# Performance work log

Measured on AMD Instinct MI355X. Metric: run time of the kernel, lower is better.

The kernel has to match this reference:

```python
import jax, jax.numpy as jnp
from jax import lax
import numpy as np

DIM = 1024
SEQ = 2048
BATCH = 2
DEPTH = 2
D_INNER = 2 * DIM          # expand=2
D_STATE = 16
D_CONV = 4
DT_RANK = DIM // 16        # ceil(dim/16) = 64
FF = 4 * DIM               # ff_mult=4
EPS = 1e-5


def rmsnorm(x, w, eps=EPS):
    return x * lax.rsqrt(jnp.mean(x * x, axis=-1, keepdims=True) + eps) * w


def layernorm(x, w, b, eps=EPS):
    mu = jnp.mean(x, axis=-1, keepdims=True)
    var = jnp.mean((x - mu) ** 2, axis=-1, keepdims=True)
    return (x - mu) * lax.rsqrt(var + eps) * w + b


def silu(x):
    return x * jax.nn.sigmoid(x)


def causal_conv1d(x, w, b):
    # x: [b, l, d], depthwise causal conv, kernel w: [d, k], bias b: [d]
    xc = jnp.transpose(x, (0, 2, 1))  # [b, d, l]
    y = lax.conv_general_dilated(
        xc, w[:, None, :], window_strides=(1,), padding=[(D_CONV - 1, 0)],
        dimension_numbers=("NCH", "OIH", "NCH"), feature_group_count=D_INNER)
    y = y + b[None, :, None]
    return jnp.transpose(y, (0, 2, 1))  # [b, l, d]


def selective_scan(u, delta, A, B, C, D):
    # u, delta: [b, l, d]; A: [d, n]; B, C: [b, l, n]; D: [d]
    def step(h, inp):
        d_t, b_t, c_t, u_t = inp                       # [b,d],[b,n],[b,n],[b,d]
        dA = jnp.exp(d_t[..., None] * A)               # [b, d, n]
        h = dA * h + (d_t * u_t)[..., None] * b_t[:, None, :]
        y = jnp.einsum("bdn,bn->bd", h, c_t)
        return h, y

    h0 = jnp.zeros((u.shape[0], A.shape[0], A.shape[1]), u.dtype)
    xs = (jnp.swapaxes(delta, 0, 1), jnp.swapaxes(B, 0, 1),
          jnp.swapaxes(C, 0, 1), jnp.swapaxes(u, 0, 1))
    _, ys = lax.scan(step, h0, xs)                     # ys: [l, b, d]
    return jnp.swapaxes(ys, 0, 1) + u * D


def mamba_mixer(h, in_w, cw, cb, xp_w, dtp_w, dtp_b, A_log, D, out_w):
    # h: [b, l, dim]
    xz = jnp.einsum("bld,ed->ble", h, in_w)            # [b, l, 2*d_inner]
    x_in, z = jnp.split(xz, 2, axis=-1)
    x_c = silu(causal_conv1d(x_in, cw, cb))            # [b, l, d_inner]
    x_dbl = jnp.einsum("ble,re->blr", x_c, xp_w)       # [b, l, dt_rank+2n]
    dt = x_dbl[..., :DT_RANK]
    B = x_dbl[..., DT_RANK:DT_RANK + D_STATE]
    C = x_dbl[..., DT_RANK + D_STATE:]
    delta = jax.nn.softplus(jnp.einsum("blr,er->ble", dt, dtp_w) + dtp_b)
    A = -jnp.exp(A_log)
    y = selective_scan(x_c, delta, A, B, C, D)
    y = y * silu(z)
    return jnp.einsum("ble,de->bld", y, out_w)         # [b, l, dim]


def setup_inputs() -> dict:
    key = jax.random.key(0)
    ks = jax.random.split(key, 16)

    def nrm(k, shape, s=0.02):
        return jax.random.normal(k, shape, dtype=jnp.float32) * s

    A_init = jnp.log(jnp.tile(jnp.arange(1, D_STATE + 1, dtype=jnp.float32),
                              (DEPTH, D_INNER, 1)))
    return {
        "x": jax.random.normal(ks[0], (BATCH, SEQ, DIM), jnp.float32),
        "in_proj_w": nrm(ks[1], (DEPTH, 2 * D_INNER, DIM)),
        "conv_w": nrm(ks[2], (DEPTH, D_INNER, D_CONV), 0.1),
        "conv_b": jnp.zeros((DEPTH, D_INNER), jnp.float32),
        "x_proj_w": nrm(ks[3], (DEPTH, DT_RANK + 2 * D_STATE, D_INNER)),
        "dt_proj_w": nrm(ks[4], (DEPTH, D_INNER, DT_RANK), 0.1),
        "dt_proj_b": nrm(ks[5], (DEPTH, D_INNER), 0.1),
        "A_log": A_init,
        "D": jnp.ones((DEPTH, D_INNER), jnp.float32),
        "out_proj_w": nrm(ks[6], (DEPTH, DIM, D_INNER)),
        "rms_w": jnp.ones((DEPTH, DIM), jnp.float32),
        "ln_w": jnp.ones((DEPTH, DIM), jnp.float32),
        "ln_b": jnp.zeros((DEPTH, DIM), jnp.float32),
        "ff_w1": nrm(ks[7], (2 * FF, DIM)),
        "ff_b1": jnp.zeros((2 * FF,), jnp.float32),
        "ff_w2": nrm(ks[8], (DIM, FF)),
        "ff_b2": jnp.zeros((DIM,), jnp.float32),
    }


def reference(x, in_proj_w, conv_w, conv_b, x_proj_w, dt_proj_w, dt_proj_b,
              A_log, D, out_proj_w, rms_w, ln_w, ln_b, ff_w1, ff_b1, ff_w2, ff_b2):
    residual = None
    h = x
    for i in range(in_proj_w.shape[0]):
        # fused add + RMSNorm (prenorm, residual in fp32)
        residual = h if residual is None else residual + h
        normed = rmsnorm(residual, rms_w[i])
        h = mamba_mixer(normed, in_proj_w[i], conv_w[i], conv_b[i],
                        x_proj_w[i], dt_proj_w[i], dt_proj_b[i],
                        A_log[i], D[i], out_proj_w[i])
        # extra per-block LayerNorm on mixer output
        h = layernorm(h, ln_w[i], ln_b[i])
    # final GEGLU feedforward
    u = jnp.einsum("bld,ed->ble", h, ff_w1) + ff_b1    # [b, l, 2*FF]
    a, g = jnp.split(u, 2, axis=-1)
    v = a * jax.nn.gelu(g, approximate=False)
    return jnp.einsum("blf,df->bld", v, ff_w2) + ff_b2
```

## Files before the change

### kernel.cpp

```cpp
#include <hip/hip_runtime.h>
#include <cstdint>
#include <cstddef>

#define DIM     1024
#define SEQ     2048
#define BATCH   2
#define DEPTH   2
#define D_INNER 2048
#define D_STATE 16
#define D_CONV  4
#define DT_RANK 64
#define FF      4096
#define ROWS    (BATCH*SEQ)
#define EPS     1e-5f

#define CS      32
#define NC      (SEQ/CS)
#define NC_LOG  6

#define XP_KS    8
#define XP_KSTEP (D_INNER/XP_KS)

#define LOG2E 1.44269504088896f

typedef unsigned short ushort_t;
typedef short bf16x8 __attribute__((ext_vector_type(8)));
typedef float f32x4  __attribute__((ext_vector_type(4)));

__device__ __forceinline__ float sigmoidf_(float x) { return 1.f / (1.f + __expf(-x)); }

__device__ __forceinline__ ushort_t f2bf(float x) {
  unsigned int u = __float_as_uint(x);
  u += 0x7fffu + ((u >> 16) & 1u);
  return (ushort_t)(u >> 16);
}
__device__ __forceinline__ float bf2f(ushort_t u) {
  return __uint_as_float((unsigned)u << 16);
}

__device__ __forceinline__ void async_cp16(const void* g, void* lds) {
  __builtin_amdgcn_global_load_lds(
      (const __attribute__((address_space(1))) unsigned int*)g,
      (__attribute__((address_space(3))) unsigned int*)lds, 16, 0, 0);
}

__device__ __forceinline__ float2 block_sum2(float a, float b) {
#pragma unroll
  for (int off = 32; off > 0; off >>= 1) {
    a += __shfl_down(a, off, 64);
    b += __shfl_down(b, off, 64);
  }
  __shared__ float sa[4], sb[4];
  __syncthreads();
  if ((threadIdx.x & 63) == 0) { int w = threadIdx.x >> 6; sa[w] = a; sb[w] = b; }
  __syncthreads();
  return make_float2(sa[0] + sa[1] + sa[2] + sa[3], sb[0] + sb[1] + sb[2] + sb[3]);
}

__global__ __launch_bounds__(256) void res_rms_kernel(
    const float* __restrict__ xin,
    float* __restrict__ res, ushort_t* __restrict__ nrm, const float* __restrict__ w) {
  int row = blockIdx.x;
  const float* xr = xin + (size_t)row * DIM;
  float* rr = res + (size_t)row * DIM;
  ushort_t* nr = nrm + (size_t)row * DIM;
  float v[4]; float ss = 0.f;
#pragma unroll
  for (int i = 0; i < 4; ++i) {
    int j = threadIdx.x + i * 256;
    float t = xr[j];
    v[i] = t; rr[j] = t; ss += t * t;
  }
  float2 s = block_sum2(ss, 0.f);
  float rstd = rsqrtf(s.x * (1.f / DIM) + EPS);
#pragma unroll
  for (int i = 0; i < 4; ++i) {
    int j = threadIdx.x + i * 256;
    nr[j] = f2bf(v[i] * rstd * w[j]);
  }
}

__global__ __launch_bounds__(256) void ln_res_rms_kernel(
    const float* __restrict__ in, float* __restrict__ res,
    const float* __restrict__ lw, const float* __restrict__ lb,
    const float* __restrict__ rw, ushort_t* __restrict__ nrm) {
  int row = blockIdx.x;
  const float* xr = in + (size_t)row * DIM;
  float* rr = res + (size_t)row * DIM;
  ushort_t* nr = nrm + (size_t)row * DIM;
  float v[4]; float s1 = 0.f, s2 = 0.f;
#pragma unroll
  for (int i = 0; i < 4; ++i) {
    int j = threadIdx.x + i * 256;
    float t = xr[j];
    v[i] = t; s1 += t; s2 += t * t;
  }
  float2 s = block_sum2(s1, s2);
  float mean = s.x * (1.f / DIM);
  float var = s.y * (1.f / DIM) - mean * mean;
  float rstd = rsqrtf(var + EPS);
  float t4[4]; float ss = 0.f;
#pragma unroll
  for (int i = 0; i < 4; ++i) {
    int j = threadIdx.x + i * 256;
    float o = (v[i] - mean) * rstd * lw[j] + lb[j];
    float t = rr[j] + o;
    rr[j] = t;
    t4[i] = t; ss += t * t;
  }
  float2 s2v = block_sum2(ss, 0.f);
  float rstd2 = rsqrtf(s2v.x * (1.f / DIM) + EPS);
#pragma unroll
  for (int i = 0; i < 4; ++i) {
    int j = threadIdx.x + i * 256;
    nr[j] = f2bf(t4[i] * rstd2 * rw[j]);
  }
}

__global__ __launch_bounds__(256) void ln_final_kernel(
    const float* __restrict__ in, ushort_t* __restrict__ outb,
    const float* __restrict__ w, const float* __restrict__ b) {
  int row = blockIdx.x;
  const float* xr = in + (size_t)row * DIM;
  ushort_t* obrow = outb + (size_t)row * DIM;
  float v[4]; float s1 = 0.f, s2 = 0.f;
#pragma unroll
  for (int i = 0; i < 4; ++i) {
    int j = threadIdx.x + i * 256;
    float t = xr[j];
    v[i] = t; s1 += t; s2 += t * t;
  }
  float2 s = block_sum2(s1, s2);
  float mean = s.x * (1.f / DIM);
  float var = s.y * (1.f / DIM) - mean * mean;
  float rstd = rsqrtf(var + EPS);
#pragma unroll
  for (int i = 0; i < 4; ++i) {
    int j = threadIdx.x + i * 256;
    obrow[j] = f2bf((v[i] - mean) * rstd * w[j] + b[j]);
  }
}

__global__ __launch_bounds__(256) void f2b_all(
    const float* __restrict__ w0, ushort_t* __restrict__ d0,
    const float* __restrict__ w1, ushort_t* __restrict__ d1,
    const float* __restrict__ w2, ushort_t* __restrict__ d2,
    const float* __restrict__ w3, ushort_t* __restrict__ d3) {
  int i = (blockIdx.x * 256 + threadIdx.x) * 4;
  const float* s; ushort_t* d; int off;
  if (i < 8388608)        { s = w0; d = d0; off = i; }
  else if (i < 12582912)  { s = w1; d = d1; off = i - 8388608; }
  else if (i < 20971520)  { s = w2; d = d2; off = i - 12582912; }
  else                    { s = w3; d = d3; off = i - 20971520; }
  float4 v = *reinterpret_cast<const float4*>(s + off);
  d[off + 0] = f2bf(v.x); d[off + 1] = f2bf(v.y);
  d[off + 2] = f2bf(v.z); d[off + 3] = f2bf(v.w);
}

__global__ __launch_bounds__(256) void gemm_bf16_nt(
    const ushort_t* __restrict__ A,
    const ushort_t* __restrict__ B,
    float* __restrict__ C,
    ushort_t* __restrict__ Cb,
    int N, int K,
    const float* __restrict__ bias, int grp) {
  __shared__ ushort_t As[2][128 * 64];
  __shared__ ushort_t Bs[2][128 * 64];
  const int tid = threadIdx.x;
  const int l = tid & 63;
  const int w = tid >> 6;

  const unsigned nwgx = gridDim.x;
  const unsigned nwg = nwgx * gridDim.y;
  const unsigned bid = blockIdx.y * nwgx + blockIdx.x;
  const unsigned cpx = nwg >> 3;
  const unsigned s = (bid & 7u) * cpx + (bid >> 3);
  const unsigned bandw = (unsigned)grp * nwgx;
  const unsigned band = s / bandw;
  const unsigned rem = s % bandw;
  const int m0 = (int)(band * grp + (rem % grp)) * 128;
  const int n0 = (int)(rem / grp) * 128;

  const int wm = (w >> 1) * 64;
  const int wn = (w & 1) * 64;

  const int srow = l >> 3;
  const int ksrc = 8 * ((l & 7) ^ srow);
  const int kg = l >> 4;
  const int lr = l & 15;

  f32x4 acc[4][4];
#pragma unroll
  for (int mi = 0; mi < 4; ++mi)
#pragma unroll
    for (int ni = 0; ni < 4; ++ni) acc[mi][ni] = (f32x4)0.f;

  const int nt = K >> 6;

#define STAGE_NT(buf, t)                                                      \
  do {                                                                        \
    int k0_ = (t) << 6;                                                       \
    _Pragma("unroll")                                                         \
    for (int j = 0; j < 4; ++j) {                                             \
      int c = j * 4 + w;                                                      \
      int r = c * 8 + srow;                                                   \
      async_cp16(&A[(size_t)(m0 + r) * K + k0_ + ksrc], &As[buf][c * 512]);   \
    }                                                                         \
    _Pragma("unroll")                                                         \
    for (int j = 0; j < 4; ++j) {                                             \
      int c = j * 4 + w;                                                      \
      int r = c * 8 + srow;                                                   \
      async_cp16(&B[(size_t)(n0 + r) * K + k0_ + ksrc], &Bs[buf][c * 512]);   \
    }                                                                         \
  } while (0)

#define COMPUTE_NT(buf)                                                       \
  do {                                                                        \
    _Pragma("unroll")                                                         \
    for (int ks = 0; ks < 2; ++ks) {                                          \
      bf16x8 af[4], bfr[4];                                                   \
      _Pragma("unroll")                                                       \
      for (int mi = 0; mi < 4; ++mi) {                                        \
        int r = wm + mi * 16 + lr;                                            \
        int boff = r * 128 + ((ks * 64 + kg * 16) ^ ((r & 7) << 4));          \
        af[mi] = *reinterpret_cast<const bf16x8*>(                            \
            reinterpret_cast<const char*>(As[buf]) + boff);                   \
      }                                                                       \
      _Pragma("unroll")                                                       \
      for (int ni = 0; ni < 4; ++ni) {                                        \
        int r = wn + ni * 16 + lr;                                            \
        int boff = r * 128 + ((ks * 64 + kg * 16) ^ ((r & 7) << 4));          \
        bfr[ni] = *reinterpret_cast<const bf16x8*>(                           \
            reinterpret_cast<const char*>(Bs[buf]) + boff);                   \
      }                                                                       \
      _Pragma("unroll")                                                       \
      for (int mi = 0; mi < 4; ++mi)                                          \
        _Pragma("unroll")                                                     \
        for (int ni = 0; ni < 4; ++ni)                                        \
          acc[mi][ni] = __builtin_amdgcn_mfma_f32_16x16x32_bf16(              \
              af[mi], bfr[ni], acc[mi][ni], 0, 0, 0);                         \
    }                                                                         \
  } while (0)

  STAGE_NT(0, 0);
  int cur = 0;
  for (int t = 0; t < nt; ++t) {
    if (t + 1 < nt) {
      STAGE_NT(cur ^ 1, t + 1);
      asm volatile("s_waitcnt vmcnt(8)" ::: "memory");
    } else {
      asm volatile("s_waitcnt vmcnt(0)" ::: "memory");
    }
    asm volatile("s_barrier" ::: "memory");
    COMPUTE_NT(cur);
    asm volatile("s_barrier" ::: "memory");
    cur ^= 1;
  }
#undef STAGE_NT
#undef COMPUTE_NT

  const int crow0 = (l >> 4) * 4;
  const int ccol = l & 15;
#pragma unroll
  for (int mi = 0; mi < 4; ++mi) {
#pragma unroll
    for (int ni = 0; ni < 4; ++ni) {
      int col = n0 + wn + ni * 16 + ccol;
      float bv = bias ? bias[col] : 0.f;
#pragma unroll
      for (int j = 0; j < 4; ++j) {
        int row = m0 + wm + mi * 16 + crow0 + j;
        float v = acc[mi][ni][j] + bv;
        if (Cb) Cb[(size_t)row * N + col] = f2bf(v);
        else    C[(size_t)row * N + col] = v;
      }
    }
  }
}

__global__ __launch_bounds__(256) void gemm_bf16_nt64(
    const ushort_t* __restrict__ A,
    const ushort_t* __restrict__ B,
    float* __restrict__ C,
    int N, int K,
    const float* __restrict__ bias, int grp) {
  __shared__ ushort_t As[2][64 * 64];
  __shared__ ushort_t Bs[2][128 * 64];
  const int tid = threadIdx.x;
  const int l = tid & 63;
  const int w = tid >> 6;

  const unsigned nwgx = gridDim.x;
  const unsigned nwg = nwgx * gridDim.y;
  const unsigned bid = blockIdx.y * nwgx + blockIdx.x;
  const unsigned cpx = nwg >> 3;
  const unsigned s = (bid & 7u) * cpx + (bid >> 3);
  const unsigned bandw = (unsigned)grp * nwgx;
  const unsigned band = s / bandw;
  const unsigned rem = s % bandw;
  const int m0 = (int)(band * grp + (rem % grp)) * 64;
  const int n0 = (int)(rem / grp) * 128;

  const int wm = (w >> 1) * 32;
  const int wn = (w & 1) * 64;

  const int srow = l >> 3;
  const int ksrc = 8 * ((l & 7) ^ srow);
  const int kg = l >> 4;
  const int lr = l & 15;

  f32x4 acc[2][4];
#pragma unroll
  for (int mi = 0; mi < 2; ++mi)
#pragma unroll
    for (int ni = 0; ni < 4; ++ni) acc[mi][ni] = (f32x4)0.f;

  const int nt = K >> 6;

#define STAGE_64(buf, t)                                                      \
  do {                                                                        \
    int k0_ = (t) << 6;                                                       \
    _Pragma("unroll")                                                         \
    for (int j = 0; j < 2; ++j) {                                             \
      int c = j * 4 + w;                                                      \
      int r = c * 8 + srow;                                                   \
      async_cp16(&A[(size_t)(m0 + r) * K + k0_ + ksrc], &As[buf][c * 512]);   \
    }                                                                         \
    _Pragma("unroll")                                                         \
    for (int j = 0; j < 4; ++j) {                                             \
      int c = j * 4 + w;                                                      \
      int r = c * 8 + srow;                                                   \
      async_cp16(&B[(size_t)(n0 + r) * K + k0_ + ksrc], &Bs[buf][c * 512]);   \
    }                                                                         \
  } while (0)

#define COMPUTE_64(buf)                                                       \
  do {                                                                        \
    _Pragma("unroll")                                                         \
    for (int ks = 0; ks < 2; ++ks) {                                          \
      bf16x8 af[2], bfr[4];                                                   \
      _Pragma("unroll")                                                       \
      for (int mi = 0; mi < 2; ++mi) {                                        \
        int r = wm + mi * 16 + lr;                                            \
        int boff = r * 128 + ((ks * 64 + kg * 16) ^ ((r & 7) << 4));          \
        af[mi] = *reinterpret_cast<const bf16x8*>(                            \
            reinterpret_cast<const char*>(As[buf]) + boff);                   \
      }                                                                       \
      _Pragma("unroll")                                                       \
      for (int ni = 0; ni < 4; ++ni) {                                        \
        int r = wn + ni * 16 + lr;                                            \
        int boff = r * 128 + ((ks * 64 + kg * 16) ^ ((r & 7) << 4));          \
        bfr[ni] = *reinterpret_cast<const bf16x8*>(                           \
            reinterpret_cast<const char*>(Bs[buf]) + boff);                   \
      }                                                                       \
      _Pragma("unroll")                                                       \
      for (int mi = 0; mi < 2; ++mi)                                          \
        _Pragma("unroll")                                                     \
        for (int ni = 0; ni < 4; ++ni)                                        \
          acc[mi][ni] = __builtin_amdgcn_mfma_f32_16x16x32_bf16(              \
              af[mi], bfr[ni], acc[mi][ni], 0, 0, 0);                         \
    }                                                                         \
  } while (0)

  STAGE_64(0, 0);
  int cur = 0;
  for (int t = 0; t < nt; ++t) {
    if (t + 1 < nt) {
      STAGE_64(cur ^ 1, t + 1);
      asm volatile("s_waitcnt vmcnt(6)" ::: "memory");
    } else {
      asm volatile("s_waitcnt vmcnt(0)" ::: "memory");
    }
    asm volatile("s_barrier" ::: "memory");
    COMPUTE_64(cur);
    asm volatile("s_barrier" ::: "memory");
    cur ^= 1;
  }
#undef STAGE_64
#undef COMPUTE_64

  const int crow0 = (l >> 4) * 4;
  const int ccol = l & 15;
#pragma unroll
  for (int mi = 0; mi < 2; ++mi) {
#pragma unroll
    for (int ni = 0; ni < 4; ++ni) {
      int col = n0 + wn + ni * 16 + ccol;
      float bv = bias ? bias[col] : 0.f;
#pragma unroll
      for (int j = 0; j < 4; ++j) {
        int row = m0 + wm + mi * 16 + crow0 + j;
        C[(size_t)row * N + col] = acc[mi][ni][j] + bv;
      }
    }
  }
}

__global__ __launch_bounds__(256) void gemm_ffn1_glu(
    const ushort_t* __restrict__ A,
    const ushort_t* __restrict__ B,
    ushort_t* __restrict__ O,
    int K,
    const float* __restrict__ bias, int grp) {
  __shared__ ushort_t As[128 * 64];
  __shared__ ushort_t Bs[128 * 64];
  const int tid = threadIdx.x;
  const int l = tid & 63;
  const int w = tid >> 6;

  const unsigned nwgx = gridDim.x;
  const unsigned nwg = nwgx * gridDim.y;
  const unsigned bid = blockIdx.y * nwgx + blockIdx.x;
  const unsigned cpx = nwg >> 3;
  const unsigned s = (bid & 7u) * cpx + (bid >> 3);
  const unsigned bandw = (unsigned)grp * nwgx;
  const unsigned band = s / bandw;
  const unsigned rem = s % bandw;
  const int m0 = (int)(band * grp + (rem % grp)) * 128;
  const int n0 = (int)(rem / grp) * 64;

  const int wm = (w >> 1) * 64;
  const int wn2 = (w & 1) * 32;

  const int srow = l >> 3;
  const int ksrc = 8 * ((l & 7) ^ srow);
  const int kg = l >> 4;
  const int lr = l & 15;

  f32x4 acc[4][4];
#pragma unroll
  for (int mi = 0; mi < 4; ++mi)
#pragma unroll
    for (int ni = 0; ni < 4; ++ni) acc[mi][ni] = (f32x4)0.f;

  for (int k0 = 0; k0 < K; k0 += 64) {
#pragma unroll
    for (int j = 0; j < 4; ++j) {
      int c = j * 4 + w;
      int r = c * 8 + srow;
      async_cp16(&A[(size_t)(m0 + r) * K + k0 + ksrc], &As[c * 512]);
    }
#pragma unroll
    for (int j = 0; j < 4; ++j) {
      int c = j * 4 + w;
      int gr = (c < 8) ? (n0 + c * 8 + srow)
                       : (FF + n0 + (c - 8) * 8 + srow);
      async_cp16(&B[(size_t)gr * K + k0 + ksrc], &Bs[c * 512]);
    }
    __syncthreads();
#pragma unroll
    for (int ks = 0; ks < 2; ++ks) {
      bf16x8 af[4], bfr[4];
#pragma unroll
      for (int mi = 0; mi < 4; ++mi) {
        int r = wm + mi * 16 + lr;
        int boff = r * 128 + ((ks * 64 + kg * 16) ^ ((r & 7) << 4));
        af[mi] = *reinterpret_cast<const bf16x8*>(reinterpret_cast<const char*>(As) + boff);
      }
#pragma unroll
      for (int ni = 0; ni < 4; ++ni) {
        int r = (ni < 2 ? wn2 + ni * 16 : 64 + wn2 + (ni - 2) * 16) + lr;
        int boff = r * 128 + ((ks * 64 + kg * 16) ^ ((r & 7) << 4));
        bfr[ni] = *reinterpret_cast<const bf16x8*>(reinterpret_cast<const char*>(Bs) + boff);
      }
#pragma unroll
      for (int mi = 0; mi < 4; ++mi)
#pragma unroll
        for (int ni = 0; ni < 4; ++ni)
          acc[mi][ni] = __builtin_amdgcn_mfma_f32_16x16x32_bf16(af[mi], bfr[ni], acc[mi][ni], 0, 0, 0);
    }
    __syncthreads();
  }

  const int crow0 = (l >> 4) * 4;
  const int ccol = l & 15;
#pragma unroll
  for (int mi = 0; mi < 4; ++mi) {
#pragma unroll
    for (int ni = 0; ni < 2; ++ni) {
      int col = n0 + wn2 + ni * 16 + ccol;
      float ba = bias[col];
      float bg = bias[FF + col];
#pragma unroll
      for (int j = 0; j < 4; ++j) {
        int row = m0 + wm + mi * 16 + crow0 + j;
        float a = acc[mi][ni][j] + ba;
        float g = acc[mi][ni + 2][j] + bg;
        float ge = 0.5f * g * (1.f + erff(g * 0.70710678118654752f));
        O[(size_t)row * FF + col] = f2bf(a * ge);
      }
    }
  }
}

__global__ __launch_bounds__(256) void gemm_nt(
    const float* __restrict__ A, int lda,
    const float* __restrict__ B, int ldb,
    ushort_t* __restrict__ Cb, int ldc,
    int N, int K,
    const float* __restrict__ bias, int act) {
  __shared__ __align__(16) float Asf[16][68];
  __shared__ __align__(16) float Bsf[16][68];
  const int tx = threadIdx.x;
  const int ty = threadIdx.y;
  const int tid = ty * 16 + tx;
  const int m0 = blockIdx.y * 64;
  const int n0 = blockIdx.x * 64;
  const int lrow = tid >> 2;
  const int lk = (tid & 3) * 4;

  float acc[4][4] = {{0.f}};

  for (int k0 = 0; k0 < K; k0 += 16) {
    float4 av, bv;
    {
      const float* ap = A + (size_t)(m0 + lrow) * lda + k0 + lk;
      av = *reinterpret_cast<const float4*>(ap);
    }
    int brow = n0 + lrow;
    if (brow < N) {
      const float* bp = B + (size_t)brow * ldb + k0 + lk;
      bv = *reinterpret_cast<const float4*>(bp);
    } else {
      bv = make_float4(0.f, 0.f, 0.f, 0.f);
    }
    __syncthreads();
    Asf[lk + 0][lrow] = av.x; Asf[lk + 1][lrow] = av.y;
    Asf[lk + 2][lrow] = av.z; Asf[lk + 3][lrow] = av.w;
    Bsf[lk + 0][lrow] = bv.x; Bsf[lk + 1][lrow] = bv.y;
    Bsf[lk + 2][lrow] = bv.z; Bsf[lk + 3][lrow] = bv.w;
    __syncthreads();
#pragma unroll
    for (int k = 0; k < 16; ++k) {
      const float4 a4 = *reinterpret_cast<const float4*>(&Asf[k][ty * 4]);
      const float4 b4 = *reinterpret_cast<const float4*>(&Bsf[k][tx * 4]);
      float a[4] = {a4.x, a4.y, a4.z, a4.w};
      float bb[4] = {b4.x, b4.y, b4.z, b4.w};
#pragma unroll
      for (int i = 0; i < 4; ++i)
#pragma unroll
        for (int j = 0; j < 4; ++j)
          acc[i][j] = fmaf(a[i], bb[j], acc[i][j]);
    }
  }

#pragma unroll
  for (int i = 0; i < 4; ++i) {
    int m = m0 + ty * 4 + i;
    int n = n0 + tx * 4;
    ushort4 ov;
    float v0 = acc[i][0], v1 = acc[i][1], v2 = acc[i][2], v3 = acc[i][3];
    if (bias) { v0 += bias[n]; v1 += bias[n + 1]; v2 += bias[n + 2]; v3 += bias[n + 3]; }
    if (act == 1) {
      v0 = (v0 > 20.f) ? v0 : log1pf(__expf(v0));
      v1 = (v1 > 20.f) ? v1 : log1pf(__expf(v1));
      v2 = (v2 > 20.f) ? v2 : log1pf(__expf(v2));
      v3 = (v3 > 20.f) ? v3 : log1pf(__expf(v3));
    }
    ov.x = f2bf(v0); ov.y = f2bf(v1); ov.z = f2bf(v2); ov.w = f2bf(v3);
    *reinterpret_cast<ushort4*>(Cb + (size_t)m * ldc + n) = ov;
  }
}

__global__ __launch_bounds__(256) void xproj_partial(
    const ushort_t* __restrict__ A,
    const float* __restrict__ W,
    float* __restrict__ pbuf) {
  __shared__ __align__(16) float As[64][68];
  __shared__ __align__(16) float Wsd[96][68];
  const int ks = blockIdx.x;
  const int mb = blockIdx.y;
  const int tid = threadIdx.x;
  const int r0 = (tid >> 4) * 4;
  const int c0 = (tid & 15) * 6;

  float acc[4][6];
#pragma unroll
  for (int i = 0; i < 4; ++i)
#pragma unroll
    for (int j = 0; j < 6; ++j) acc[i][j] = 0.f;

  for (int k0 = 0; k0 < XP_KSTEP; k0 += 64) {
    const int kbase = ks * XP_KSTEP + k0;
    __syncthreads();
    {
      int r = tid >> 2, c = (tid & 3) * 16;
      const ushort_t* src = A + (size_t)(mb * 64 + r) * D_INNER + kbase + c;
#pragma unroll
      for (int q = 0; q < 4; ++q) {
        ushort4 uv = *reinterpret_cast<const ushort4*>(src + q * 4);
        As[r][c + q * 4 + 0] = bf2f(uv.x);
        As[r][c + q * 4 + 1] = bf2f(uv.y);
        As[r][c + q * 4 + 2] = bf2f(uv.z);
        As[r][c + q * 4 + 3] = bf2f(uv.w);
      }
    }
#pragma unroll
    for (int q = 0; q < 6; ++q) {
      int f = q * 256 + tid;
      int wr = f >> 4;
      int wc = (f & 15) * 4;
      *reinterpret_cast<float4*>(&Wsd[wr][wc]) =
          *reinterpret_cast<const float4*>(&W[(size_t)wr * D_INNER + kbase + wc]);
    }
    __syncthreads();
#pragma unroll 16
    for (int k = 0; k < 64; ++k) {
      float a[4], wv[6];
#pragma unroll
      for (int i = 0; i < 4; ++i) a[i] = As[r0 + i][k];
#pragma unroll
      for (int j = 0; j < 6; ++j) wv[j] = Wsd[c0 + j][k];
#pragma unroll
      for (int i = 0; i < 4; ++i)
#pragma unroll
        for (int j = 0; j < 6; ++j)
          acc[i][j] = fmaf(a[i], wv[j], acc[i][j]);
    }
  }

  float* dst = pbuf + ((size_t)ks * ROWS + mb * 64) * 96;
#pragma unroll
  for (int i = 0; i < 4; ++i)
#pragma unroll
    for (int j = 0; j < 6; ++j)
      dst[(size_t)(r0 + i) * 96 + c0 + j] = acc[i][j];
}

__global__ __launch_bounds__(256) void xproj_reduce(
    const float* __restrict__ pbuf, float* __restrict__ xdbl) {
  int i = blockIdx.x * 256 + threadIdx.x;
  float s = 0.f;
#pragma unroll
  for (int ks = 0; ks < XP_KS; ++ks)
    s += pbuf[(size_t)ks * (ROWS * 96) + i];
  xdbl[i] = s;
}

__global__ __launch_bounds__(256) void conv_silu_kernel(
    const ushort_t* __restrict__ xzb, ushort_t* __restrict__ xcb,
    const float* __restrict__ cw, const float* __restrict__ cb) {
  int t = (blockIdx.x * 256 + threadIdx.x) * 4;
  if (t >= ROWS * D_INNER) return;
  int d = t & (D_INNER - 1);
  int row = t >> 11;
  int l = row & (SEQ - 1);
  float acc[4];
#pragma unroll
  for (int q = 0; q < 4; ++q) acc[q] = cb[d + q];
#pragma unroll
  for (int j = 0; j < 4; ++j) {
    int ls = l - 3 + j;
    if (ls >= 0) {
      ushort4 uv = *reinterpret_cast<const ushort4*>(
          xzb + (size_t)(row - 3 + j) * (2 * D_INNER) + d);
      acc[0] = fmaf(cw[(d + 0) * 4 + j], bf2f(uv.x), acc[0]);
      acc[1] = fmaf(cw[(d + 1) * 4 + j], bf2f(uv.y), acc[1]);
      acc[2] = fmaf(cw[(d + 2) * 4 + j], bf2f(uv.z), acc[2]);
      acc[3] = fmaf(cw[(d + 3) * 4 + j], bf2f(uv.w), acc[3]);
    }
  }
  ushort4 o;
  o.x = f2bf(acc[0] * sigmoidf_(acc[0]));
  o.y = f2bf(acc[1] * sigmoidf_(acc[1]));
  o.z = f2bf(acc[2] * sigmoidf_(acc[2]));
  o.w = f2bf(acc[3] * sigmoidf_(acc[3]));
  *reinterpret_cast<ushort4*>(xcb + t) = o;
}

__global__ __launch_bounds__(256) void scan_pass1(
    const ushort_t* __restrict__ delta,
    const ushort_t* __restrict__ xcb,
    const float* __restrict__ xdbl,
    const float* __restrict__ A_log,
    float* __restrict__ harr,
    float* __restrict__ dtsum) {
  __shared__ __align__(16) float Bls[CS][16];
  int gid = blockIdx.x * 256 + threadIdx.x;
  int d = gid & (D_INNER - 1);
  int bc = gid >> 11;
  int c = bc & (NC - 1);
  int b = bc >> NC_LOG;
  const size_t r0 = (size_t)b * SEQ + (size_t)c * CS;

  if (threadIdx.x < CS * 4) {
    int sl = threadIdx.x >> 2, sf = (threadIdx.x & 3) * 4;
    *reinterpret_cast<f32x4*>(&Bls[sl][sf]) =
        *reinterpret_cast<const f32x4*>(xdbl + (r0 + sl) * 96 + 64 + sf);
  }

  float Av2[D_STATE];
#pragma unroll
  for (int n = 0; n < D_STATE; ++n)
    Av2[n] = -__expf(A_log[(size_t)d * D_STATE + n]) * LOG2E;
  float h[D_STATE];
#pragma unroll
  for (int n = 0; n < D_STATE; ++n) h[n] = 0.f;
  float dts = 0.f;

  const ushort_t* drow = delta + r0 * D_INNER + d;
  const ushort_t* urow = xcb + r0 * D_INNER + d;

  float pdt[4], pu[4];
#pragma unroll
  for (int g = 0; g < 4; ++g) {
    pdt[g] = bf2f(drow[(size_t)g * D_INNER]);
    pu[g]  = bf2f(urow[(size_t)g * D_INNER]);
  }
  __syncthreads();

  for (int l0 = 0; l0 < CS; l0 += 4) {
    float cdt[4], cu[4];
#pragma unroll
    for (int g = 0; g < 4; ++g) { cdt[g] = pdt[g]; cu[g] = pu[g]; }
    if (l0 + 4 < CS) {
#pragma unroll
      for (int g = 0; g < 4; ++g) {
        pdt[g] = bf2f(drow[(size_t)(l0 + 4 + g) * D_INNER]);
        pu[g]  = bf2f(urow[(size_t)(l0 + 4 + g) * D_INNER]);
      }
    }
#pragma unroll
    for (int g = 0; g < 4; ++g) {
      int l = l0 + g;
      f32x4 B0 = *reinterpret_cast<const f32x4*>(&Bls[l][0]);
      f32x4 B1 = *reinterpret_cast<const f32x4*>(&Bls[l][4]);
      f32x4 B2 = *reinterpret_cast<const f32x4*>(&Bls[l][8]);
      f32x4 B3 = *reinterpret_cast<const f32x4*>(&Bls[l][12]);
      float du = cdt[g] * cu[g];
      dts += cdt[g];
      float Bsr[D_STATE] = {B0[0],B0[1],B0[2],B0[3], B1[0],B1[1],B1[2],B1[3],
                            B2[0],B2[1],B2[2],B2[3], B3[0],B3[1],B3[2],B3[3]};
#pragma unroll
      for (int n = 0; n < D_STATE; ++n) {
        float dA = __builtin_amdgcn_exp2f(cdt[g] * Av2[n]);
        h[n] = dA * h[n] + du * Bsr[n];
      }
    }
  }
#pragma unroll
  for (int n = 0; n < D_STATE; ++n)
    harr[((size_t)bc * D_STATE + n) * D_INNER + d] = h[n];
  dtsum[(size_t)bc * D_INNER + d] = dts;
}

__global__ __launch_bounds__(256) void scan_pass2(
    float* __restrict__ harr,
    const float* __restrict__ dtsum,
    const float* __restrict__ A_log) {
  int gid = blockIdx.x * 256 + threadIdx.x;
  int d = gid & (D_INNER - 1);
  int bn = gid >> 11;
  int n = bn & (D_STATE - 1);
  int b = bn >> 4;
  float Av2 = -__expf(A_log[(size_t)d * D_STATE + n]) * LOG2E;
  float h = 0.f;
  for (int c = 0; c < NC; ++c) {
    size_t bc = (size_t)b * NC + c;
    size_t idx = (bc * D_STATE + n) * D_INNER + d;
    float he = harr[idx];
    harr[idx] = h;
    float P = __builtin_amdgcn_exp2f(Av2 * dtsum[bc * D_INNER + d]);
    h = P * h + he;
  }
}

__global__ __launch_bounds__(256) void scan_pass3(
    const ushort_t* __restrict__ delta,
    const ushort_t* __restrict__ xcb,
    ushort_t* __restrict__ ybf,
    const float* __restrict__ xdbl,
    const ushort_t* __restrict__ xzb,
    const float* __restrict__ A_log,
    const float* __restrict__ Dp,
    const float* __restrict__ harr) {
  __shared__ __align__(16) float BCls[CS][32];
  int gid = blockIdx.x * 256 + threadIdx.x;
  int d = gid & (D_INNER - 1);
  int bc = gid >> 11;
  int c = bc & (NC - 1);
  int b = bc >> NC_LOG;
  const size_t r0 = (size_t)b * SEQ + (size_t)c * CS;

  {
    int sl = threadIdx.x >> 3, sf = (threadIdx.x & 7) * 4;
    *reinterpret_cast<f32x4*>(&BCls[sl][sf]) =
        *reinterpret_cast<const f32x4*>(xdbl + (r0 + sl) * 96 + 64 + sf);
  }

  float Av2[D_STATE];
#pragma unroll
  for (int n = 0; n < D_STATE; ++n)
    Av2[n] = -__expf(A_log[(size_t)d * D_STATE + n]) * LOG2E;
  const float Dd = Dp[d];
  float h[D_STATE];
#pragma unroll
  for (int n = 0; n < D_STATE; ++n)
    h[n] = harr[((size_t)bc * D_STATE + n) * D_INNER + d];

  const ushort_t* drow = delta + r0 * D_INNER + d;
  const ushort_t* urow = xcb + r0 * D_INNER + d;
  const ushort_t* zrow = xzb + r0 * (2 * D_INNER) + D_INNER + d;
  ushort_t* yrow = ybf + r0 * D_INNER + d;

  float pdt[4], pu[4], pz[4];
#pragma unroll
  for (int g = 0; g < 4; ++g) {
    pdt[g] = bf2f(drow[(size_t)g * D_INNER]);
    pu[g]  = bf2f(urow[(size_t)g * D_INNER]);
    pz[g]  = bf2f(zrow[(size_t)g * (2 * D_INNER)]);
  }
  __syncthreads();

  for (int l0 = 0; l0 < CS; l0 += 4) {
    float cdt[4], cu[4], cz[4];
#pragma unroll
    for (int g = 0; g < 4; ++g) { cdt[g] = pdt[g]; cu[g] = pu[g]; cz[g] = pz[g]; }
    if (l0 + 4 < CS) {
#pragma unroll
      for (int g = 0; g < 4; ++g) {
        pdt[g] = bf2f(drow[(size_t)(l0 + 4 + g) * D_INNER]);
        pu[g]  = bf2f(urow[(size_t)(l0 + 4 + g) * D_INNER]);
        pz[g]  = bf2f(zrow[(size_t)(l0 + 4 + g) * (2 * D_INNER)]);
      }
    }
#pragma unroll
    for (int g = 0; g < 4; ++g) {
      int l = l0 + g;
      f32x4 B0 = *reinterpret_cast<const f32x4*>(&BCls[l][0]);
      f32x4 B1 = *reinterpret_cast<const f32x4*>(&BCls[l][4]);
      f32x4 B2 = *reinterpret_cast<const f32x4*>(&BCls[l][8]);
      f32x4 B3 = *reinterpret_cast<const f32x4*>(&BCls[l][12]);
      f32x4 C0 = *reinterpret_cast<const f32x4*>(&BCls[l][16]);
      f32x4 C1 = *reinterpret_cast<const f32x4*>(&BCls[l][20]);
      f32x4 C2 = *reinterpret_cast<const f32x4*>(&BCls[l][24]);
      f32x4 C3 = *reinterpret_cast<const f32x4*>(&BCls[l][28]);
      float du = cdt[g] * cu[g];
      float Bsr[D_STATE] = {B0[0],B0[1],B0[2],B0[3], B1[0],B1[1],B1[2],B1[3],
                            B2[0],B2[1],B2[2],B2[3], B3[0],B3[1],B3[2],B3[3]};
      float Csr[D_STATE] = {C0[0],C0[1],C0[2],C0[3], C1[0],C1[1],C1[2],C1[3],
                            C2[0],C2[1],C2[2],C2[3], C3[0],C3[1],C3[2],C3[3]};
      float y = 0.f;
#pragma unroll
      for (int n = 0; n < D_STATE; ++n) {
        float dA = __builtin_amdgcn_exp2f(cdt[g] * Av2[n]);
        h[n] = dA * h[n] + du * Bsr[n];
        y = fmaf(h[n], Csr[n], y);
      }
      y = fmaf(cu[g], Dd, y);
      yrow[(size_t)l * D_INNER] = f2bf(y * (cz[g] * sigmoidf_(cz[g])));
    }
  }
}

extern "C" void kernel_launch(void* const* d_in, const int* in_sizes, int n_in,
                              void* d_out, int out_size, void* d_ws, size_t ws_size,
                              hipStream_t stream) {
  const float* x         = (const float*)d_in[0];
  const float* in_proj_w = (const float*)d_in[1];
  const float* conv_w    = (const float*)d_in[2];
  const float* conv_b    = (const float*)d_in[3];
  const float* x_proj_w  = (const float*)d_in[4];
  const float* dt_proj_w = (const float*)d_in[5];
  const float* dt_proj_b = (const float*)d_in[6];
  const float* A_log     = (const float*)d_in[7];
  const float* Dp        = (const float*)d_in[8];
  const float* out_proj_w= (const float*)d_in[9];
  const float* rms_w     = (const float*)d_in[10];
  const float* ln_w      = (const float*)d_in[11];
  const float* ln_b      = (const float*)d_in[12];
  const float* ff_w1     = (const float*)d_in[13];
  const float* ff_b1     = (const float*)d_in[14];
  const float* ff_w2     = (const float*)d_in[15];
  const float* ff_b2     = (const float*)d_in[16];
  float* out = (float*)d_out;

  float* ws = (float*)d_ws;
  float* res     = ws;
  float* dtsum   = ws + 4194304;
  float* xdbl    = ws + 8388608;
  ushort_t* hbuf_bf = (ushort_t*)(ws + 8912896);
  float*    pbuf    = ws + 11010048;
  ushort_t* y_bf    = (ushort_t*)(ws + 15204352);
  ushort_t* glu_bf  = (ushort_t*)(ws + 11010048);
  float* big   = ws + 19398656;
  ushort_t* xz_bf = (ushort_t*)big;
  ushort_t* xcb   = (ushort_t*)(big + 8388608);
  ushort_t* delta_bf = (ushort_t*)(big + 16777216);
  float* harr  = big + 25165824;
  float* op_out= big;
  ushort_t* nrm_bf = (ushort_t*)(big + 16777216 + 4194304);
  ushort_t* in_w_bf  = (ushort_t*)(ws + 52953088);
  ushort_t* out_w_bf = (ushort_t*)(ws + 57147392);
  ushort_t* ff1_bf   = (ushort_t*)(ws + 59244544);
  ushort_t* ff2_bf   = (ushort_t*)(ws + 63438848);

  dim3 tb(16, 16);

  f2b_all<<<24576, 256, 0, stream>>>(in_proj_w, in_w_bf, out_proj_w, out_w_bf,
                                     ff_w1, ff1_bf, ff_w2, ff2_bf);

  res_rms_kernel<<<ROWS, 256, 0, stream>>>(x, res, nrm_bf, rms_w);

  for (int i = 0; i < DEPTH; ++i) {
    const float* cw    = conv_w + (size_t)i * D_INNER * D_CONV;
    const float* cb    = conv_b + (size_t)i * D_INNER;
    const float* xp_w  = x_proj_w + (size_t)i * 96 * D_INNER;
    const float* dtp_w = dt_proj_w + (size_t)i * D_INNER * DT_RANK;
    const float* dtp_b = dt_proj_b + (size_t)i * D_INNER;
    const float* Alg   = A_log + (size_t)i * D_INNER * D_STATE;
    const float* Di    = Dp + (size_t)i * D_INNER;

    gemm_bf16_nt<<<dim3(32, 32), 256, 0, stream>>>(
        nrm_bf, in_w_bf + (size_t)i * 4194304, nullptr, xz_bf, 2 * D_INNER, DIM,
        nullptr, 16);
    conv_silu_kernel<<<(ROWS * D_INNER / 4) / 256, 256, 0, stream>>>(xz_bf, xcb, cw, cb);
    xproj_partial<<<dim3(XP_KS, 64), 256, 0, stream>>>(xcb, xp_w, pbuf);
    xproj_reduce<<<(ROWS * 96) / 256, 256, 0, stream>>>(pbuf, xdbl);
    gemm_nt<<<dim3(32, 64), tb, 0, stream>>>(xdbl, 96, dtp_w, DT_RANK, delta_bf,
                                             D_INNER, D_INNER, DT_RANK, dtp_b, 1);
    scan_pass1<<<(BATCH * NC * D_INNER) / 256, 256, 0, stream>>>(delta_bf, xcb, xdbl,
                                                                 Alg, harr, dtsum);
    scan_pass2<<<(BATCH * D_STATE * D_INNER) / 256, 256, 0, stream>>>(harr, dtsum, Alg);
    scan_pass3<<<(BATCH * NC * D_INNER) / 256, 256, 0, stream>>>(delta_bf, xcb, y_bf,
                                                                 xdbl, xz_bf, Alg, Di,
                                                                 harr);
    gemm_bf16_nt64<<<dim3(8, 64), 256, 0, stream>>>(
        y_bf, out_w_bf + (size_t)i * 2097152, op_out, DIM, D_INNER, nullptr, 8);
    if (i + 1 < DEPTH) {
      ln_res_rms_kernel<<<ROWS, 256, 0, stream>>>(
          op_out, res, ln_w + (size_t)i * DIM, ln_b + (size_t)i * DIM,
          rms_w + (size_t)(i + 1) * DIM, nrm_bf);
    } else {
      ln_final_kernel<<<ROWS, 256, 0, stream>>>(
          op_out, hbuf_bf, ln_w + (size_t)i * DIM, ln_b + (size_t)i * DIM);
    }
  }

  gemm_ffn1_glu<<<dim3(64, 32), 256, 0, stream>>>(hbuf_bf, ff1_bf, glu_bf, DIM,
                                                  ff_b1, 16);
  gemm_bf16_nt64<<<dim3(8, 64), 256, 0, stream>>>(glu_bf, ff2_bf, out, DIM, FF,
                                                  ff_b2, 8);
}
```

Before: 735.1 us.

## Double-buffer FFN1 GLU GEMM loads and halve the N tile

```diff
diff --git a/kernel.cpp b/kernel.cpp
--- a/kernel.cpp
+++ b/kernel.cpp
@@ -402,8 +402,8 @@
     ushort_t* __restrict__ O,
     int K,
     const float* __restrict__ bias, int grp) {
-  __shared__ ushort_t As[128 * 64];
-  __shared__ ushort_t Bs[128 * 64];
+  __shared__ ushort_t As[2][128 * 64];
+  __shared__ ushort_t Bs[2][64 * 64];
   const int tid = threadIdx.x;
   const int l = tid & 63;
   const int w = tid >> 6;
@@ -417,78 +417,101 @@
   const unsigned band = s / bandw;
   const unsigned rem = s % bandw;
   const int m0 = (int)(band * grp + (rem % grp)) * 128;
-  const int n0 = (int)(rem / grp) * 64;
+  const int n0 = (int)(rem / grp) * 32;
 
   const int wm = (w >> 1) * 64;
-  const int wn2 = (w & 1) * 32;
+  const int wn2 = (w & 1) * 16;
 
   const int srow = l >> 3;
   const int ksrc = 8 * ((l & 7) ^ srow);
   const int kg = l >> 4;
   const int lr = l & 15;
 
-  f32x4 acc[4][4];
+  f32x4 acc[4][2];
 #pragma unroll
   for (int mi = 0; mi < 4; ++mi)
 #pragma unroll
-    for (int ni = 0; ni < 4; ++ni) acc[mi][ni] = (f32x4)0.f;
-
-  for (int k0 = 0; k0 < K; k0 += 64) {
-#pragma unroll
-    for (int j = 0; j < 4; ++j) {
-      int c = j * 4 + w;
-      int r = c * 8 + srow;
-      async_cp16(&A[(size_t)(m0 + r) * K + k0 + ksrc], &As[c * 512]);
-    }
-#pragma unroll
-    for (int j = 0; j < 4; ++j) {
-      int c = j * 4 + w;
-      int gr = (c < 8) ? (n0 + c * 8 + srow)
-                       : (FF + n0 + (c - 8) * 8 + srow);
-      async_cp16(&B[(size_t)gr * K + k0 + ksrc], &Bs[c * 512]);
-    }
-    __syncthreads();
-#pragma unroll
-    for (int ks = 0; ks < 2; ++ks) {
-      bf16x8 af[4], bfr[4];
-#pragma unroll
-      for (int mi = 0; mi < 4; ++mi) {
-        int r = wm + mi * 16 + lr;
-        int boff = r * 128 + ((ks * 64 + kg * 16) ^ ((r & 7) << 4));
-        af[mi] = *reinterpret_cast<const bf16x8*>(reinterpret_cast<const char*>(As) + boff);
-      }
-#pragma unroll
-      for (int ni = 0; ni < 4; ++ni) {
-        int r = (ni < 2 ? wn2 + ni * 16 : 64 + wn2 + (ni - 2) * 16) + lr;
-        int boff = r * 128 + ((ks * 64 + kg * 16) ^ ((r & 7) << 4));
-        bfr[ni] = *reinterpret_cast<const bf16x8*>(reinterpret_cast<const char*>(Bs) + boff);
-      }
-#pragma unroll
-      for (int mi = 0; mi < 4; ++mi)
-#pragma unroll
-        for (int ni = 0; ni < 4; ++ni)
-          acc[mi][ni] = __builtin_amdgcn_mfma_f32_16x16x32_bf16(af[mi], bfr[ni], acc[mi][ni], 0, 0, 0);
-    }
-    __syncthreads();
-  }
+    for (int ni = 0; ni < 2; ++ni) acc[mi][ni] = (f32x4)0.f;
+
+  const int nt = K >> 6;
+
+#define STAGE_FG(buf, t)                                                      \
+  do {                                                                        \
+    int k0_ = (t) << 6;                                                       \
+    _Pragma("unroll")                                                         \
+    for (int j = 0; j < 4; ++j) {                                             \
+      int c = j * 4 + w;                                                      \
+      int r = c * 8 + srow;                                                   \
+      async_cp16(&A[(size_t)(m0 + r) * K + k0_ + ksrc], &As[buf][c * 512]);   \
+    }                                                                         \
+    _Pragma("unroll")                                                         \
+    for (int j = 0; j < 2; ++j) {                                             \
+      int c = j * 4 + w;                                                      \
+      int gr = (c < 4) ? (n0 + c * 8 + srow)                                  \
+                       : (FF + n0 + (c - 4) * 8 + srow);                      \
+      async_cp16(&B[(size_t)gr * K + k0_ + ksrc], &Bs[buf][c * 512]);         \
+    }                                                                         \
+  } while (0)
+
+#define COMPUTE_FG(buf)                                                       \
+  do {                                                                        \
+    _Pragma("unroll")                                                         \
+    for (int ks = 0; ks < 2; ++ks) {                                          \
+      bf16x8 af[4], bfr[2];                                                   \
+      _Pragma("unroll")                                                       \
+      for (int mi = 0; mi < 4; ++mi) {                                        \
+        int r = wm + mi * 16 + lr;                                            \
+        int boff = r * 128 + ((ks * 64 + kg * 16) ^ ((r & 7) << 4));          \
+        af[mi] = *reinterpret_cast<const bf16x8*>(                            \
+            reinterpret_cast<const char*>(As[buf]) + boff);                   \
+      }                                                                       \
+      _Pragma("unroll")                                                       \
+      for (int ni = 0; ni < 2; ++ni) {                                        \
+        int r = ni * 32 + wn2 + lr;                                           \
+        int boff = r * 128 + ((ks * 64 + kg * 16) ^ ((r & 7) << 4));          \
+        bfr[ni] = *reinterpret_cast<const bf16x8*>(                           \
+            reinterpret_cast<const char*>(Bs[buf]) + boff);                   \
+      }                                                                       \
+      _Pragma("unroll")                                                       \
+      for (int mi = 0; mi < 4; ++mi)                                          \
+        _Pragma("unroll")                                                     \
+        for (int ni = 0; ni < 2; ++ni)                                        \
+          acc[mi][ni] = __builtin_amdgcn_mfma_f32_16x16x32_bf16(              \
+              af[mi], bfr[ni], acc[mi][ni], 0, 0, 0);                         \
+    }                                                                         \
+  } while (0)
+
+  STAGE_FG(0, 0);
+  int cur = 0;
+  for (int t = 0; t < nt; ++t) {
+    if (t + 1 < nt) {
+      STAGE_FG(cur ^ 1, t + 1);
+      asm volatile("s_waitcnt vmcnt(6)" ::: "memory");
+    } else {
+      asm volatile("s_waitcnt vmcnt(0)" ::: "memory");
+    }
+    asm volatile("s_barrier" ::: "memory");
+    COMPUTE_FG(cur);
+    asm volatile("s_barrier" ::: "memory");
+    cur ^= 1;
+  }
+#undef STAGE_FG
+#undef COMPUTE_FG
 
   const int crow0 = (l >> 4) * 4;
   const int ccol = l & 15;
 #pragma unroll
   for (int mi = 0; mi < 4; ++mi) {
-#pragma unroll
-    for (int ni = 0; ni < 2; ++ni) {
-      int col = n0 + wn2 + ni * 16 + ccol;
-      float ba = bias[col];
-      float bg = bias[FF + col];
-#pragma unroll
-      for (int j = 0; j < 4; ++j) {
-        int row = m0 + wm + mi * 16 + crow0 + j;
-        float a = acc[mi][ni][j] + ba;
-        float g = acc[mi][ni + 2][j] + bg;
-        float ge = 0.5f * g * (1.f + erff(g * 0.70710678118654752f));
-        O[(size_t)row * FF + col] = f2bf(a * ge);
-      }
+    int col = n0 + wn2 + ccol;
+    float ba = bias[col];
+    float bg = bias[FF + col];
+#pragma unroll
+    for (int j = 0; j < 4; ++j) {
+      int row = m0 + wm + mi * 16 + crow0 + j;
+      float a = acc[mi][0][j] + ba;
+      float g = acc[mi][1][j] + bg;
+      float ge = 0.5f * g * (1.f + erff(g * 0.70710678118654752f));
+      O[(size_t)row * FF + col] = f2bf(a * ge);
     }
   }
 }
@@ -937,8 +960,8 @@
     }
   }
 
-  gemm_ffn1_glu<<<dim3(64, 32), 256, 0, stream>>>(hbuf_bf, ff1_bf, glu_bf, DIM,
-                                                  ff_b1, 16);
+  gemm_ffn1_glu<<<dim3(128, 32), 256, 0, stream>>>(hbuf_bf, ff1_bf, glu_bf, DIM,
+                                                   ff_b1, 16);
   gemm_bf16_nt64<<<dim3(8, 64), 256, 0, stream>>>(glu_bf, ff2_bf, out, DIM, FF,
                                                   ff_b2, 8);
 }
```

Measured after the change: 748.2 us. About the same (+1.8%).
